# Kernel optimization log

Measured on AMD Instinct MI355X. Metric: run time of the kernel, lower is better.

## Reference

```python
import jax, jax.numpy as jnp
import numpy as np

B, T, D, H = 2, 2048, 1024, 16
HD = D // H

def setup_inputs() -> dict:
    key = jax.random.key(0)
    ks = jax.random.split(key, 5)
    fan = D
    bound_w = float(np.sqrt(6.0 / fan))  # kaiming_uniform-ish scale
    return {
        "x": jax.random.normal(ks[0], (B, T, D), dtype=jnp.float32),
        "W_qkv": jax.random.uniform(ks[1], (3 * D, D), minval=-bound_w, maxval=bound_w, dtype=jnp.float32),
        "b_qkv": jax.random.uniform(ks[2], (3 * D,), minval=-bound_w, maxval=bound_w, dtype=jnp.float32),
        "W_proj": jax.random.uniform(ks[3], (D, D), minval=-bound_w, maxval=bound_w, dtype=jnp.float32),
        "b_proj": jax.random.uniform(ks[4], (D,), minval=-bound_w, maxval=bound_w, dtype=jnp.float32),
    }

def reference(x, W_qkv, b_qkv, W_proj, b_proj):
    Bx, Tx, C = x.shape
    h, hd = H, C // H
    qkv = x @ W_qkv.T + b_qkv                      # (B,T,3C)
    q, k, v = jnp.split(qkv, 3, axis=-1)
    # (B,T,C) -> (B,h,T,hd)
    q = q.reshape(Bx, Tx, h, hd).transpose(0, 2, 1, 3)
    k = k.reshape(Bx, Tx, h, hd).transpose(0, 2, 1, 3)
    v = v.reshape(Bx, Tx, h, hd).transpose(0, 2, 1, 3)
    scale = hd ** -0.5
    scores = jnp.einsum('bhqd,bhkd->bhqk', q, k) * scale
    causal = jnp.tril(jnp.ones((Tx, Tx), dtype=bool))
    scores = jnp.where(causal, scores, -jnp.inf)
    weights = jax.nn.softmax(scores, axis=-1)      # stable softmax, same math
    out = jnp.einsum('bhqk,bhkd->bhqd', weights, v)
    out = out.transpose(0, 2, 1, 3).reshape(Bx, Tx, C)
    return out @ W_proj.T + b_proj
```

## Files before the change

kernel.cpp:

```cpp
#include <hip/hip_runtime.h>

typedef unsigned short u16;
typedef __attribute__((ext_vector_type(8))) short bf16x8;
typedef __attribute__((ext_vector_type(4))) float f32x4;

#define Bb 2
#define Tt 2048
#define Dd 1024
#define Hh 16
#define HD 64
#define NTOK (Bb*Tt)
#define QKVN (3*Dd)

__device__ __forceinline__ u16 f2b(float f) {
    unsigned u = __float_as_uint(f);
    unsigned r = (u + 0x7fffu + ((u >> 16) & 1u)) >> 16;
    return (u16)r;
}

__device__ __forceinline__ void g2l16(const u16* g, u16* l) {
    __builtin_amdgcn_global_load_lds(
        (const __attribute__((address_space(1))) unsigned int*)g,
        (__attribute__((address_space(3))) unsigned int*)l,
        16, 0, 0);
}

__device__ __forceinline__ unsigned pk2(float lo, float hi) {
    return __builtin_amdgcn_perm(__float_as_uint(hi), __float_as_uint(lo), 0x07060302u);
}

#define N4X  (NTOK * Dd / 4)
#define N4WQ (3 * Dd * Dd / 4)
#define N4WP (Dd * Dd / 4)
__global__ void cvt_all(const float* __restrict__ x, const float* __restrict__ wq,
                        const float* __restrict__ wp, u16* __restrict__ xb,
                        u16* __restrict__ wqb, u16* __restrict__ wpb) {
    int i = blockIdx.x * blockDim.x + threadIdx.x;
    const float* src; u16* dst; int j;
    if (i < N4X)                { src = x;  dst = xb;  j = i; }
    else if (i < N4X + N4WQ)    { src = wq; dst = wqb; j = i - N4X; }
    else                        { src = wp; dst = wpb; j = i - N4X - N4WQ; }
    float4 f = ((const float4*)src)[j];
    ushort4 o;
    o.x = f2b(f.x); o.y = f2b(f.y); o.z = f2b(f.z); o.w = f2b(f.w);
    ((ushort4*)dst)[j] = o;
}

#define TRS 136

__global__ __launch_bounds__(256, 2)
void gemm_qkv(const u16* __restrict__ A, const u16* __restrict__ Bt,
              const float* __restrict__ bias,
              u16* __restrict__ C16, u16* __restrict__ Vt) {
    const int N = QKVN, K = Dd;
    __shared__ alignas(16) u16 smem[128 * TRS];
    u16* As = smem;
    u16* Bs = smem + 8192;
    const int tid = threadIdx.x;
    const int wave = tid >> 6, lane = tid & 63;
    const int quad = lane >> 4, l16 = lane & 15;
    const int wm = (wave & 1) * 64, wn = (wave >> 1) * 64;
    const int m0 = blockIdx.x * 128, n0 = blockIdx.y * 128;
    const int lrow = lane >> 2, lcol = (lane & 3) << 3;

    f32x4 acc[4][4];
#pragma unroll
    for (int i = 0; i < 4; ++i)
#pragma unroll
        for (int j = 0; j < 4; ++j)
            acc[i][j] = (f32x4){0.f, 0.f, 0.f, 0.f};

    for (int k0 = 0; k0 < K; k0 += 64) {
#pragma unroll
        for (int h = 0; h < 2; ++h)
#pragma unroll
            for (int c = 0; c < 2; ++c) {
                const int rb = (c * 4 + wave) * 16;
                g2l16(A  + (size_t)(m0 + rb + lrow) * K + k0 + h * 32 + lcol,
                      &As[h * 4096 + rb * 32 + (lane << 3)]);
                g2l16(Bt + (size_t)(n0 + rb + lrow) * K + k0 + h * 32 + lcol,
                      &Bs[h * 4096 + rb * 32 + (lane << 3)]);
            }
        __syncthreads();
        bf16x8 a[4][2], b[4][2];
#pragma unroll
        for (int h = 0; h < 2; ++h) {
#pragma unroll
            for (int i = 0; i < 4; ++i)
                a[i][h] = *(const bf16x8*)(&As[h * 4096 + (wm + i * 16 + l16) * 32 + quad * 8]);
#pragma unroll
            for (int i = 0; i < 4; ++i)
                b[i][h] = *(const bf16x8*)(&Bs[h * 4096 + (wn + i * 16 + l16) * 32 + quad * 8]);
        }
#pragma unroll
        for (int h = 0; h < 2; ++h)
#pragma unroll
            for (int i = 0; i < 4; ++i)
#pragma unroll
                for (int j = 0; j < 4; ++j)
                    acc[i][j] = __builtin_amdgcn_mfma_f32_16x16x32_bf16(a[i][h], b[j][h], acc[i][j], 0, 0, 0);
        __syncthreads();
    }

    float b4[4];
#pragma unroll
    for (int j = 0; j < 4; ++j) b4[j] = bias[n0 + wn + j * 16 + l16];
    const bool isV = (n0 >= 2 * Dd);

    if (!isV) {
#pragma unroll
        for (int i = 0; i < 4; ++i)
#pragma unroll
            for (int j = 0; j < 4; ++j)
#pragma unroll
                for (int r = 0; r < 4; ++r) {
                    int m = m0 + wm + i * 16 + quad * 4 + r;
                    int n = n0 + wn + j * 16 + l16;
                    C16[(size_t)m * N + n] = f2b(acc[i][j][r] + b4[j]);
                }
    } else {
#pragma unroll
        for (int i = 0; i < 4; ++i)
#pragma unroll
            for (int j = 0; j < 4; ++j)
#pragma unroll
                for (int r = 0; r < 4; ++r) {
                    int ml = wm + i * 16 + quad * 4 + r;
                    int nl = wn + j * 16 + l16;
                    smem[nl * TRS + ml] = f2b(acc[i][j][r] + b4[j]);
                }
        __syncthreads();
        const int bidx = m0 >> 11, t0 = m0 & 2047;
        const int nl = tid >> 1, toff = (tid & 1) * 64;
        u16* dst = Vt + (size_t)bidx * (Hh * HD * Tt)
                      + (size_t)(n0 - 2 * Dd + nl) * Tt + t0 + toff;
        const u16* srcl = &smem[nl * TRS + toff];
#pragma unroll
        for (int k = 0; k < 8; ++k)
            *(uint4*)(dst + k * 8) = *(const uint4*)(srcl + k * 8);
    }
}

__global__ __launch_bounds__(256, 2)
void gemm_proj(const u16* __restrict__ A, const u16* __restrict__ Bt,
               const float* __restrict__ bias, float* __restrict__ Co) {
    const int N = Dd, K = Dd;
    __shared__ alignas(16) u16 As[2 * 128 * 32];
    __shared__ alignas(16) u16 Bs[2 * 64 * 32];
    const int tid = threadIdx.x;
    const int wave = tid >> 6, lane = tid & 63;
    const int quad = lane >> 4, l16 = lane & 15;
    const int wm = (wave & 1) * 64, wn = (wave >> 1) * 32;
    const int m0 = blockIdx.x * 128, n0 = blockIdx.y * 64;
    const int lrow = lane >> 2, lcol = (lane & 3) << 3;

    f32x4 acc[4][2];
#pragma unroll
    for (int i = 0; i < 4; ++i)
#pragma unroll
        for (int j = 0; j < 2; ++j)
            acc[i][j] = (f32x4){0.f, 0.f, 0.f, 0.f};

    for (int k0 = 0; k0 < K; k0 += 64) {
#pragma unroll
        for (int h = 0; h < 2; ++h) {
#pragma unroll
            for (int c = 0; c < 2; ++c) {
                const int rb = (c * 4 + wave) * 16;
                g2l16(A + (size_t)(m0 + rb + lrow) * K + k0 + h * 32 + lcol,
                      &As[h * 4096 + rb * 32 + (lane << 3)]);
            }
            g2l16(Bt + (size_t)(n0 + wave * 16 + lrow) * K + k0 + h * 32 + lcol,
                  &Bs[h * 2048 + (wave * 16) * 32 + (lane << 3)]);
        }
        __syncthreads();
        bf16x8 a[4][2], b[2][2];
#pragma unroll
        for (int h = 0; h < 2; ++h) {
#pragma unroll
            for (int i = 0; i < 4; ++i)
                a[i][h] = *(const bf16x8*)(&As[h * 4096 + (wm + i * 16 + l16) * 32 + quad * 8]);
#pragma unroll
            for (int j = 0; j < 2; ++j)
                b[j][h] = *(const bf16x8*)(&Bs[h * 2048 + (wn + j * 16 + l16) * 32 + quad * 8]);
        }
#pragma unroll
        for (int h = 0; h < 2; ++h)
#pragma unroll
            for (int i = 0; i < 4; ++i)
#pragma unroll
                for (int j = 0; j < 2; ++j)
                    acc[i][j] = __builtin_amdgcn_mfma_f32_16x16x32_bf16(a[i][h], b[j][h], acc[i][j], 0, 0, 0);
        __syncthreads();
    }

    float b2[2];
#pragma unroll
    for (int j = 0; j < 2; ++j) b2[j] = bias[n0 + wn + j * 16 + l16];

#pragma unroll
    for (int i = 0; i < 4; ++i)
#pragma unroll
        for (int j = 0; j < 2; ++j)
#pragma unroll
            for (int r = 0; r < 4; ++r) {
                int m = m0 + wm + i * 16 + quad * 4 + r;
                int n = n0 + wn + j * 16 + l16;
                Co[(size_t)m * N + n] = acc[i][j][r] + b2[j];
            }
}

#define LKP 80
#define PSP 84
#define FMX 24.0f

__global__ __launch_bounds__(256, 3)
void attn_fwd(const u16* __restrict__ qkv, const u16* __restrict__ Vt,
              u16* __restrict__ Ao) {
    const int pair = blockIdx.x, bh = blockIdx.y;
    const int hh = bh & (Hh - 1), bidx = bh >> 4;
    const u16* Qp = qkv + (size_t)bidx * Tt * QKVN + hh * HD;
    const u16* Kp = Qp + Dd;
    const u16* Vp = Vt + (size_t)bh * HD * Tt;
    const int tid = threadIdx.x;
    const int wave = tid >> 6, lane = tid & 63;
    const int quad = lane >> 4, l16 = lane & 15;

    __shared__ alignas(16) u16 Ks[2][64 * LKP];
    __shared__ alignas(16) u16 Vs[2][64 * LKP];
    __shared__ alignas(16) u16 Ps[4][16 * PSP];
    u16* Pw = &Ps[wave][0];

    const int srow = tid >> 3, scol = (tid & 7) << 3;
    const float sc = 0.125f * 1.44269504f;

    for (int half = 0; half < 2; ++half) {
        const int qt = half ? pair : (31 - pair);
        const int q0 = qt * 64;
        const int qrow_g = q0 + wave * 16 + l16;
        bf16x8 aq[2];
#pragma unroll
        for (int kk = 0; kk < 2; ++kk)
            aq[kk] = *(const bf16x8*)(Qp + (size_t)qrow_g * QKVN + kk * 32 + quad * 8);

        f32x4 o[4];
#pragma unroll
        for (int nt = 0; nt < 4; ++nt) o[nt] = (f32x4){0.f, 0.f, 0.f, 0.f};
        float lsum = 0.f;
        const int nit = qt + 1;

        {
            uint4 k0r = *(const uint4*)(Kp + (size_t)srow * QKVN + scol);
            uint4 k1r = *(const uint4*)(Kp + (size_t)(srow + 32) * QKVN + scol);
            uint4 v0r = *(const uint4*)(Vp + (size_t)srow * Tt + scol);
            uint4 v1r = *(const uint4*)(Vp + (size_t)(srow + 32) * Tt + scol);
            *(uint4*)(&Ks[0][srow * LKP + scol]) = k0r;
            *(uint4*)(&Ks[0][(srow + 32) * LKP + scol]) = k1r;
            *(uint4*)(&Vs[0][srow * LKP + scol]) = v0r;
            *(uint4*)(&Vs[0][(srow + 32) * LKP + scol]) = v1r;
        }
        __syncthreads();

        for (int kt = 0; kt < nit; ++kt) {
            const int cur = kt & 1;
            const u16* Kc = &Ks[cur][0];
            const u16* Vc = &Vs[cur][0];
            uint4 k0r, k1r, v0r, v1r;
            const bool more = (kt + 1 < nit);
            if (more) {
                const int kn = (kt + 1) * 64;
                k0r = *(const uint4*)(Kp + (size_t)(kn + srow) * QKVN + scol);
                k1r = *(const uint4*)(Kp + (size_t)(kn + srow + 32) * QKVN + scol);
                v0r = *(const uint4*)(Vp + (size_t)srow * Tt + kn + scol);
                v1r = *(const uint4*)(Vp + (size_t)(srow + 32) * Tt + kn + scol);
            }

            f32x4 s[4];
#pragma unroll
            for (int nt = 0; nt < 4; ++nt) {
                f32x4 z = (f32x4){0.f, 0.f, 0.f, 0.f};
#pragma unroll
                for (int kk = 0; kk < 2; ++kk) {
                    bf16x8 ak = *(const bf16x8*)(&Kc[(nt * 16 + l16) * LKP + kk * 32 + quad * 8]);
                    z = __builtin_amdgcn_mfma_f32_16x16x32_bf16(ak, aq[kk], z, 0, 0, 0);
                }
                s[nt] = z;
            }

            if (kt == qt) {
                const int k0 = kt * 64;
#pragma unroll
                for (int nt = 0; nt < 4; ++nt)
#pragma unroll
                    for (int r = 0; r < 4; ++r) {
                        int key = k0 + nt * 16 + quad * 4 + r;
                        float t = __builtin_fmaf(s[nt][r], sc, -FMX);
                        t = (key <= qrow_g) ? t : -200.0f;
                        float p = exp2f(t);
                        s[nt][r] = p;
                        lsum += p;
                    }
            } else {
#pragma unroll
                for (int nt = 0; nt < 4; ++nt)
#pragma unroll
                    for (int r = 0; r < 4; ++r) {
                        float p = exp2f(__builtin_fmaf(s[nt][r], sc, -FMX));
                        s[nt][r] = p;
                        lsum += p;
                    }
            }

#pragma unroll
            for (int nt = 0; nt < 4; ++nt) {
                uint2 d;
                d.x = pk2(s[nt][0], s[nt][1]);
                d.y = pk2(s[nt][2], s[nt][3]);
                *(uint2*)(&Pw[l16 * PSP + nt * 16 + quad * 4]) = d;
            }

#pragma unroll
            for (int kk = 0; kk < 2; ++kk) {
                bf16x8 bp = *(const bf16x8*)(&Pw[l16 * PSP + kk * 32 + quad * 8]);
#pragma unroll
                for (int nt = 0; nt < 4; ++nt) {
                    bf16x8 av = *(const bf16x8*)(&Vc[(nt * 16 + l16) * LKP + kk * 32 + quad * 8]);
                    o[nt] = __builtin_amdgcn_mfma_f32_16x16x32_bf16(av, bp, o[nt], 0, 0, 0);
                }
            }

            if (more) {
                const int nxt = cur ^ 1;
                *(uint4*)(&Ks[nxt][srow * LKP + scol]) = k0r;
                *(uint4*)(&Ks[nxt][(srow + 32) * LKP + scol]) = k1r;
                *(uint4*)(&Vs[nxt][srow * LKP + scol]) = v0r;
                *(uint4*)(&Vs[nxt][(srow + 32) * LKP + scol]) = v1r;
            }
            __syncthreads();
        }

        lsum += __shfl_xor(lsum, 16, 64);
        lsum += __shfl_xor(lsum, 32, 64);
        const float rinv = 1.0f / lsum;
        u16* orow = Ao + ((size_t)bidx * Tt + qrow_g) * Dd + hh * HD;
#pragma unroll
        for (int nt = 0; nt < 4; ++nt) {
            ushort4 p4;
            p4.x = f2b(o[nt][0] * rinv); p4.y = f2b(o[nt][1] * rinv);
            p4.z = f2b(o[nt][2] * rinv); p4.w = f2b(o[nt][3] * rinv);
            *(ushort4*)(orow + nt * 16 + quad * 4) = p4;
        }
    }
}

extern "C" void kernel_launch(void* const* d_in, const int* in_sizes, int n_in,
                              void* d_out, int out_size, void* d_ws, size_t ws_size,
                              hipStream_t stream) {
    const float* x      = (const float*)d_in[0];
    const float* W_qkv  = (const float*)d_in[1];
    const float* b_qkv  = (const float*)d_in[2];
    const float* W_proj = (const float*)d_in[3];
    const float* b_proj = (const float*)d_in[4];
    float* out = (float*)d_out;

    char* ws = (char*)d_ws;
    u16* Wprojb = (u16*)(ws);
    u16* Wqkvb  = (u16*)(ws + (2u << 20));
    u16* xb     = (u16*)(ws + (8u << 20));
    u16* qkvb   = (u16*)(ws + (16u << 20));
    u16* Vtb    = (u16*)(ws + (40u << 20));
    u16* attnb  = (u16*)(ws + (2u << 20));

    cvt_all<<<(N4X + N4WQ + N4WP) / 256, 256, 0, stream>>>(x, W_qkv, W_proj, xb, Wqkvb, Wprojb);

    {
        dim3 grid(NTOK / 128, QKVN / 128);
        gemm_qkv<<<grid, 256, 0, stream>>>(xb, Wqkvb, b_qkv, qkvb, Vtb);
    }
    {
        dim3 grid(16, Bb * Hh);
        attn_fwd<<<grid, 256, 0, stream>>>(qkvb, Vtb, attnb);
    }
    {
        dim3 grid(NTOK / 128, Dd / 64);
        gemm_proj<<<grid, 256, 0, stream>>>(attnb, Wprojb, b_proj, out);
    }
}
```

Baseline: 185.5 us.

## Process both causal query tiles concurrently in 512-thread attention blocks sharing K/V tiles

The attention kernel now runs the high and low query tiles of a pair at the same time with 8 waves, instead of one after the other with 4 waves. Each K/V tile is loaded into shared memory once and used by both halves, so the prefix that both tiles need is no longer loaded twice. The causal mask is precomputed into a per-lane bias array, and the block index order is reversed for half the heads to balance work across the grid. The low-query waves sit idle for the remaining iterations, and the launch bounds change for both the QKV GEMM and attention, which may increase register pressure.

```diff
diff --git a/kernel.cpp b/kernel.cpp
--- a/kernel.cpp
+++ b/kernel.cpp
@@ -48,7 +48,7 @@
 
 #define TRS 136
 
-__global__ __launch_bounds__(256, 2)
+__global__ __launch_bounds__(256, 3)
 void gemm_qkv(const u16* __restrict__ A, const u16* __restrict__ Bt,
               const float* __restrict__ bias,
               u16* __restrict__ C16, u16* __restrict__ Vt) {
@@ -213,11 +213,57 @@
 #define LKP 80
 #define PSP 84
 #define FMX 24.0f
-
-__global__ __launch_bounds__(256, 3)
+#define MFMA16(a,b,c) __builtin_amdgcn_mfma_f32_16x16x32_bf16(a, b, c, 0, 0, 0)
+
+template<bool MASK>
+__device__ __forceinline__ void tile_iter(
+    const u16* Kcur, const u16* Vcur, u16* Pw,
+    const bf16x8 (&aq)[2], f32x4 (&o)[4], float& lsum,
+    const float (&mb)[16], int l16, int quad, float sc)
+{
+    f32x4 s[4];
+#pragma unroll
+    for (int nt = 0; nt < 4; ++nt) {
+        f32x4 z = (f32x4){0.f, 0.f, 0.f, 0.f};
+#pragma unroll
+        for (int kk = 0; kk < 2; ++kk) {
+            bf16x8 ak = *(const bf16x8*)(&Kcur[(nt * 16 + l16) * LKP + kk * 32 + quad * 8]);
+            z = MFMA16(ak, aq[kk], z);
+        }
+        s[nt] = z;
+    }
+#pragma unroll
+    for (int nt = 0; nt < 4; ++nt)
+#pragma unroll
+        for (int r = 0; r < 4; ++r) {
+            float p = exp2f(__builtin_fmaf(s[nt][r], sc, MASK ? mb[nt * 4 + r] : -FMX));
+            s[nt][r] = p;
+            lsum += p;
+        }
+#pragma unroll
+    for (int nt = 0; nt < 4; ++nt) {
+        uint2 d;
+        d.x = pk2(s[nt][0], s[nt][1]);
+        d.y = pk2(s[nt][2], s[nt][3]);
+        *(uint2*)(&Pw[l16 * PSP + nt * 16 + quad * 4]) = d;
+    }
+#pragma unroll
+    for (int kk = 0; kk < 2; ++kk) {
+        bf16x8 bp = *(const bf16x8*)(&Pw[l16 * PSP + kk * 32 + quad * 8]);
+#pragma unroll
+        for (int nt = 0; nt < 4; ++nt) {
+            bf16x8 av = *(const bf16x8*)(&Vcur[(nt * 16 + l16) * LKP + kk * 32 + quad * 8]);
+            o[nt] = MFMA16(av, bp, o[nt]);
+        }
+    }
+}
+
+__global__ __launch_bounds__(512, 4)
 void attn_fwd(const u16* __restrict__ qkv, const u16* __restrict__ Vt,
               u16* __restrict__ Ao) {
-    const int pair = blockIdx.x, bh = blockIdx.y;
+    const int p = ((int)blockIdx.y < 16) ? (int)blockIdx.x : 15 - (int)blockIdx.x;
+    const int qtH = 31 - p, qtL = p;
+    const int bh = blockIdx.y;
     const int hh = bh & (Hh - 1), bidx = bh >> 4;
     const u16* Qp = qkv + (size_t)bidx * Tt * QKVN + hh * HD;
     const u16* Kp = Qp + Dd;
@@ -225,131 +271,87 @@
     const int tid = threadIdx.x;
     const int wave = tid >> 6, lane = tid & 63;
     const int quad = lane >> 4, l16 = lane & 15;
+    const int w4 = wave & 3;
+    const bool isH = wave < 4;
+    const int myqt = isH ? qtH : qtL;
 
     __shared__ alignas(16) u16 Ks[2][64 * LKP];
     __shared__ alignas(16) u16 Vs[2][64 * LKP];
-    __shared__ alignas(16) u16 Ps[4][16 * PSP];
+    __shared__ alignas(16) u16 Ps[8][16 * PSP];
     u16* Pw = &Ps[wave][0];
 
     const int srow = tid >> 3, scol = (tid & 7) << 3;
+    const int st = srow * LKP + scol;
     const float sc = 0.125f * 1.44269504f;
 
-    for (int half = 0; half < 2; ++half) {
-        const int qt = half ? pair : (31 - pair);
-        const int q0 = qt * 64;
-        const int qrow_g = q0 + wave * 16 + l16;
-        bf16x8 aq[2];
-#pragma unroll
-        for (int kk = 0; kk < 2; ++kk)
-            aq[kk] = *(const bf16x8*)(Qp + (size_t)qrow_g * QKVN + kk * 32 + quad * 8);
-
-        f32x4 o[4];
-#pragma unroll
-        for (int nt = 0; nt < 4; ++nt) o[nt] = (f32x4){0.f, 0.f, 0.f, 0.f};
-        float lsum = 0.f;
-        const int nit = qt + 1;
-
-        {
-            uint4 k0r = *(const uint4*)(Kp + (size_t)srow * QKVN + scol);
-            uint4 k1r = *(const uint4*)(Kp + (size_t)(srow + 32) * QKVN + scol);
-            uint4 v0r = *(const uint4*)(Vp + (size_t)srow * Tt + scol);
-            uint4 v1r = *(const uint4*)(Vp + (size_t)(srow + 32) * Tt + scol);
-            *(uint4*)(&Ks[0][srow * LKP + scol]) = k0r;
-            *(uint4*)(&Ks[0][(srow + 32) * LKP + scol]) = k1r;
-            *(uint4*)(&Vs[0][srow * LKP + scol]) = v0r;
-            *(uint4*)(&Vs[0][(srow + 32) * LKP + scol]) = v1r;
-        }
-        __syncthreads();
-
-        for (int kt = 0; kt < nit; ++kt) {
-            const int cur = kt & 1;
-            const u16* Kc = &Ks[cur][0];
-            const u16* Vc = &Vs[cur][0];
-            uint4 k0r, k1r, v0r, v1r;
-            const bool more = (kt + 1 < nit);
-            if (more) {
-                const int kn = (kt + 1) * 64;
-                k0r = *(const uint4*)(Kp + (size_t)(kn + srow) * QKVN + scol);
-                k1r = *(const uint4*)(Kp + (size_t)(kn + srow + 32) * QKVN + scol);
-                v0r = *(const uint4*)(Vp + (size_t)srow * Tt + kn + scol);
-                v1r = *(const uint4*)(Vp + (size_t)(srow + 32) * Tt + kn + scol);
-            }
-
-            f32x4 s[4];
-#pragma unroll
-            for (int nt = 0; nt < 4; ++nt) {
-                f32x4 z = (f32x4){0.f, 0.f, 0.f, 0.f};
-#pragma unroll
-                for (int kk = 0; kk < 2; ++kk) {
-                    bf16x8 ak = *(const bf16x8*)(&Kc[(nt * 16 + l16) * LKP + kk * 32 + quad * 8]);
-                    z = __builtin_amdgcn_mfma_f32_16x16x32_bf16(ak, aq[kk], z, 0, 0, 0);
-                }
-                s[nt] = z;
-            }
-
-            if (kt == qt) {
-                const int k0 = kt * 64;
-#pragma unroll
-                for (int nt = 0; nt < 4; ++nt)
-#pragma unroll
-                    for (int r = 0; r < 4; ++r) {
-                        int key = k0 + nt * 16 + quad * 4 + r;
-                        float t = __builtin_fmaf(s[nt][r], sc, -FMX);
-                        t = (key <= qrow_g) ? t : -200.0f;
-                        float p = exp2f(t);
-                        s[nt][r] = p;
-                        lsum += p;
-                    }
-            } else {
-#pragma unroll
-                for (int nt = 0; nt < 4; ++nt)
-#pragma unroll
-                    for (int r = 0; r < 4; ++r) {
-                        float p = exp2f(__builtin_fmaf(s[nt][r], sc, -FMX));
-                        s[nt][r] = p;
-                        lsum += p;
-                    }
-            }
-
-#pragma unroll
-            for (int nt = 0; nt < 4; ++nt) {
-                uint2 d;
-                d.x = pk2(s[nt][0], s[nt][1]);
-                d.y = pk2(s[nt][2], s[nt][3]);
-                *(uint2*)(&Pw[l16 * PSP + nt * 16 + quad * 4]) = d;
-            }
-
-#pragma unroll
-            for (int kk = 0; kk < 2; ++kk) {
-                bf16x8 bp = *(const bf16x8*)(&Pw[l16 * PSP + kk * 32 + quad * 8]);
-#pragma unroll
-                for (int nt = 0; nt < 4; ++nt) {
-                    bf16x8 av = *(const bf16x8*)(&Vc[(nt * 16 + l16) * LKP + kk * 32 + quad * 8]);
-                    o[nt] = __builtin_amdgcn_mfma_f32_16x16x32_bf16(av, bp, o[nt], 0, 0, 0);
-                }
-            }
-
-            if (more) {
-                const int nxt = cur ^ 1;
-                *(uint4*)(&Ks[nxt][srow * LKP + scol]) = k0r;
-                *(uint4*)(&Ks[nxt][(srow + 32) * LKP + scol]) = k1r;
-                *(uint4*)(&Vs[nxt][srow * LKP + scol]) = v0r;
-                *(uint4*)(&Vs[nxt][(srow + 32) * LKP + scol]) = v1r;
-            }
-            __syncthreads();
-        }
-
-        lsum += __shfl_xor(lsum, 16, 64);
-        lsum += __shfl_xor(lsum, 32, 64);
-        const float rinv = 1.0f / lsum;
-        u16* orow = Ao + ((size_t)bidx * Tt + qrow_g) * Dd + hh * HD;
-#pragma unroll
-        for (int nt = 0; nt < 4; ++nt) {
-            ushort4 p4;
-            p4.x = f2b(o[nt][0] * rinv); p4.y = f2b(o[nt][1] * rinv);
-            p4.z = f2b(o[nt][2] * rinv); p4.w = f2b(o[nt][3] * rinv);
-            *(ushort4*)(orow + nt * 16 + quad * 4) = p4;
-        }
+    float mb[16];
+#pragma unroll
+    for (int nt = 0; nt < 4; ++nt)
+#pragma unroll
+        for (int r = 0; r < 4; ++r)
+            mb[nt * 4 + r] = (nt * 16 + quad * 4 + r <= w4 * 16 + l16) ? -FMX : -250.0f;
+
+    const int qrow_g = myqt * 64 + w4 * 16 + l16;
+    bf16x8 aq[2];
+#pragma unroll
+    for (int kk = 0; kk < 2; ++kk)
+        aq[kk] = *(const bf16x8*)(Qp + (size_t)qrow_g * QKVN + kk * 32 + quad * 8);
+
+    f32x4 o[4];
+#pragma unroll
+    for (int nt = 0; nt < 4; ++nt) o[nt] = (f32x4){0.f, 0.f, 0.f, 0.f};
+    float lsum = 0.f;
+
+    {
+        uint4 kr = *(const uint4*)(Kp + (size_t)srow * QKVN + scol);
+        uint4 vr = *(const uint4*)(Vp + (size_t)srow * Tt + scol);
+        *(uint4*)(&Ks[0][st]) = kr;
+        *(uint4*)(&Vs[0][st]) = vr;
+    }
+    __syncthreads();
+
+    const u16* kp = Kp + (size_t)(64 + srow) * QKVN + scol;
+    const u16* vp = Vp + (size_t)srow * Tt + 64 + scol;
+    u16* Kcur = &Ks[0][0]; u16* Knxt = &Ks[1][0];
+    u16* Vcur = &Vs[0][0]; u16* Vnxt = &Vs[1][0];
+
+#define PREFETCH \
+    uint4 kr = *(const uint4*)kp; uint4 vr = *(const uint4*)vp; \
+    kp += (size_t)64 * QKVN; vp += 64;
+
+#define STAGE_SWAP \
+    *(uint4*)(&Knxt[st]) = kr; *(uint4*)(&Vnxt[st]) = vr; \
+    { u16* t = Kcur; Kcur = Knxt; Knxt = t; t = Vcur; Vcur = Vnxt; Vnxt = t; } \
+    __syncthreads();
+
+    for (int kt = 0; kt < qtL; ++kt) {
+        PREFETCH
+        tile_iter<false>(Kcur, Vcur, Pw, aq, o, lsum, mb, l16, quad, sc);
+        STAGE_SWAP
+    }
+    {
+        PREFETCH
+        if (isH) tile_iter<false>(Kcur, Vcur, Pw, aq, o, lsum, mb, l16, quad, sc);
+        else     tile_iter<true>(Kcur, Vcur, Pw, aq, o, lsum, mb, l16, quad, sc);
+        STAGE_SWAP
+    }
+    for (int kt = qtL + 1; kt < qtH; ++kt) {
+        PREFETCH
+        if (isH) tile_iter<false>(Kcur, Vcur, Pw, aq, o, lsum, mb, l16, quad, sc);
+        STAGE_SWAP
+    }
+    if (isH) tile_iter<true>(Kcur, Vcur, Pw, aq, o, lsum, mb, l16, quad, sc);
+
+    lsum += __shfl_xor(lsum, 16, 64);
+    lsum += __shfl_xor(lsum, 32, 64);
+    const float rinv = 1.0f / lsum;
+    u16* orow = Ao + ((size_t)bidx * Tt + qrow_g) * Dd + hh * HD;
+#pragma unroll
+    for (int nt = 0; nt < 4; ++nt) {
+        ushort4 p4;
+        p4.x = f2b(o[nt][0] * rinv); p4.y = f2b(o[nt][1] * rinv);
+        p4.z = f2b(o[nt][2] * rinv); p4.w = f2b(o[nt][3] * rinv);
+        *(ushort4*)(orow + nt * 16 + quad * 4) = p4;
     }
 }
 
@@ -379,7 +381,7 @@
     }
     {
         dim3 grid(16, Bb * Hh);
-        attn_fwd<<<grid, 256, 0, stream>>>(qkvb, Vtb, attnb);
+        attn_fwd<<<grid, 512, 0, stream>>>(qkvb, Vtb, attnb);
     }
     {
         dim3 grid(NTOK / 128, Dd / 64);
```

Result: no change. 183.6 us (-1.0%).
